# Kernel tuning notes

Measured on AMD Instinct MI355X. Metric: run time of the kernel, lower is better.

## Reference

```python
import jax, jax.numpy as jnp
import numpy as np

B, S, H, E, V, OOV = 64, 400, 512, 256, 50000, 100

def setup_inputs() -> dict:
    key = jax.random.key(0)
    ks = jax.random.split(key, 32)
    p = lambda i, shape: jax.random.normal(ks[i], shape, jnp.float32) * 0.02
    emb = p(0, (V, E)).at[0].set(0.0)  # padding_idx=0
    return dict(
        summaries_in=jax.random.randint(ks[1], (B,), 1, V),
        h0=jax.random.normal(ks[2], (B, H), jnp.float32),
        c0=jax.random.normal(ks[3], (B, H), jnp.float32),
        encoder_out=jax.random.normal(ks[4], (B, S, 2 * H), jnp.float32),
        encoder_features=jax.random.normal(ks[5], (S * B, 2 * H), jnp.float32),
        encoder_mask=jnp.ones((S, B), jnp.float32),
        context=jax.random.normal(ks[6], (B, 2 * H), jnp.float32),
        coverage=jax.random.uniform(ks[7], (S, B), jnp.float32) * 0.01,
        texts_extended=jax.random.randint(ks[8], (S, B), 0, V + OOV),
        oov_size=OOV,
        emb=emb,
        W_feat=p(10, (2 * H, 2 * H)), b_feat=p(11, (2 * H,)),
        W_cov=p(12, (2 * H,)), b_cov=p(13, (2 * H,)),
        w_att=p(14, (2 * H,)), b_att=p(15, ()),
        W_ih=p(16, (4 * H, E)), W_hh=p(17, (4 * H, H)),
        b_ih=p(18, (4 * H,)), b_hh=p(19, (4 * H,)),
        W_ctx=p(20, (E, 2 * H + E)), b_ctx=p(21, (E,)),
        W_pg=p(22, (4 * H + E,)), b_pg=p(23, ()),
        W_o1=p(24, (H, 3 * H)), b_o1=p(25, (H,)),
        W_o2=p(26, (V, H)), b_o2=p(27, (V,)),
    )


def reference(summaries_in, h0, c0, encoder_out, encoder_features, encoder_mask,
              context, coverage, texts_extended, oov_size, emb,
              W_feat, b_feat, W_cov, b_cov, w_att, b_att,
              W_ih, W_hh, b_ih, b_hh, W_ctx, b_ctx, W_pg, b_pg,
              W_o1, b_o1, W_o2, b_o2):
    # embedding + context projection: [B, 2H+E] -> [B, E]
    x = emb[summaries_in]
    ctx_out = jnp.concatenate([context, x], axis=1) @ W_ctx.T + b_ctx
    # single LSTM step (torch gate order i, f, g, o)
    gates = ctx_out @ W_ih.T + b_ih + h0 @ W_hh.T + b_hh
    i, f, g, o = jnp.split(gates, 4, axis=1)
    c = jax.nn.sigmoid(f) * c0 + jax.nn.sigmoid(i) * jnp.tanh(g)
    h = jax.nn.sigmoid(o) * jnp.tanh(c)
    hidden_out = jnp.concatenate([h, c], axis=1)  # [B, 2H]
    # Bahdanau attention with coverage
    dec_feat = hidden_out @ W_feat.T + b_feat                 # [B, 2H]
    ef = encoder_features.reshape(S, B, 2 * H)                # [S, B, 2H]
    cov_feat = coverage[..., None] * W_cov + b_cov            # Linear(1, 2H)
    e = jnp.tanh(ef + dec_feat[None] + cov_feat) @ w_att + b_att  # [S, B]
    a = jax.nn.softmax(e, axis=0) * encoder_mask
    a = a / jnp.sum(a, axis=0, keepdims=True)                 # renormalize (Normalize(0))
    ctx_new = jnp.einsum('sb,bsd->bd', a, encoder_out)        # [B, 2H]
    coverage_next = coverage + a
    # pointer-generator mix
    gen_in = jnp.concatenate([ctx_new, hidden_out, ctx_out], axis=1)  # [B, 4H+E]
    p_gen = jax.nn.sigmoid(gen_in @ W_pg + b_pg)[:, None]             # [B, 1]
    logits = (jnp.concatenate([h, ctx_new], axis=1) @ W_o1.T + b_o1) @ W_o2.T + b_o2
    vocab_dist = p_gen * jax.nn.softmax(logits, axis=1)       # [B, V]
    attn_w = (1.0 - p_gen) * a.T                              # [B, S]
    vd = jnp.concatenate([vocab_dist, jnp.zeros((B, oov_size), vocab_dist.dtype)], axis=1)
    vd = vd.at[jnp.arange(B)[:, None], texts_extended.T].add(attn_w)  # scatter_add copy dist
    return vd, hidden_out, ctx_new, a, coverage_next
```

## Files before the change

kernel.cpp:

```cpp
#include <hip/hip_runtime.h>
#include <cmath>

#define B 64
#define S 400
#define H 512
#define E 256
#define V 50000
#define OOV 100
#define H2 1024
#define VDN (V + OOV)
#define NBLK_V 782
#define SC 8

typedef __attribute__((ext_vector_type(8))) short short8;
typedef __attribute__((ext_vector_type(4))) float f32x4;

__device__ __forceinline__ float wred_sum(float v) {
#pragma unroll
  for (int o = 32; o > 0; o >>= 1) v += __shfl_down(v, o, 64);
  return v;
}
__device__ __forceinline__ float wred_max(float v) {
#pragma unroll
  for (int o = 32; o > 0; o >>= 1) v = fmaxf(v, __shfl_down(v, o, 64));
  return v;
}
__device__ __forceinline__ short f2bf(float f) {
  return __builtin_bit_cast(short, (__bf16)f);
}
__device__ __forceinline__ float ftanh(float x) {
  float e = __expf(2.f * x);
  return 1.f - 2.f * __builtin_amdgcn_rcpf(e + 1.f);
}
__device__ __forceinline__ float fsig(float x) {
  return __builtin_amdgcn_rcpf(1.f + __expf(-x));
}

__global__ __launch_bounds__(256) void k_pre(
    const float* __restrict__ b_ctx, const float* __restrict__ b_ih,
    const float* __restrict__ b_hh, const float* __restrict__ b_feat,
    const float* __restrict__ b_o1, const float* __restrict__ context,
    const float* __restrict__ emb, const int* __restrict__ sumin,
    const float* __restrict__ h0, float* __restrict__ ctxoutT4,
    float* __restrict__ gates, float* __restrict__ dfeat,
    float* __restrict__ innerT4, float* __restrict__ catT4,
    float* __restrict__ h0T4) {
  int idx = blockIdx.x * 256 + threadIdx.x;
  if (idx < 16384) {
    int j = ((idx >> 8) << 2) + (idx & 3);
    ctxoutT4[idx] = b_ctx[j];
  } else if (idx < 16384 + 131072) {
    int i = idx - 16384;
    int j = i & 2047;
    gates[i] = b_ih[j] + b_hh[j];
  } else if (idx < 16384 + 131072 + 65536) {
    int i = idx - 16384 - 131072;
    dfeat[i] = b_feat[i & 1023];
  } else if (idx < 245760) {
    int i = idx - 16384 - 131072 - 65536;
    int j = ((i >> 8) << 2) + (i & 3);
    innerT4[i] = b_o1[j];
  } else if (idx < 245760 + 81920) {
    int i = idx - 245760;
    int e = i & 3, b = (i >> 2) & 63, q = i >> 8;
    int k = q * 4 + e;
    catT4[i] = (k < 1024) ? context[b * 1024 + k]
                          : emb[(size_t)sumin[b] * 256 + (k - 1024)];
  } else {
    int i = idx - 245760 - 81920;
    int e = i & 3, b = (i >> 2) & 63, q = i >> 8;
    h0T4[i] = h0[b * 512 + q * 4 + e];
  }
}

template <int R, int KC, int OUTMODE>
__global__ __launch_bounds__(256) void k_gemmsk(
    const float* __restrict__ A1, const float* __restrict__ W1, int ldw1, int s1,
    const float* __restrict__ A2, const float* __restrict__ W2, int ldw2,
    float* __restrict__ out, int ldout) {
  const int lane = threadIdx.x;
  const int w = threadIdx.y;
  const int j0 = blockIdx.x * (4 * R) + w * R;
  const float* A;
  const float* W;
  int ldw, kc0;
  if ((int)blockIdx.y < s1) {
    A = A1; W = W1; ldw = ldw1; kc0 = blockIdx.y * KC;
  } else {
    A = A2; W = W2; ldw = ldw2; kc0 = (blockIdx.y - s1) * KC;
  }
  float acc[R];
#pragma unroll
  for (int r = 0; r < R; ++r) acc[r] = 0.f;
  const float* ap = A + (size_t)kc0 * 256 + lane * 4;
  const float* wr[R];
#pragma unroll
  for (int r = 0; r < R; ++r) wr[r] = W + (size_t)(j0 + r) * ldw + kc0 * 4;
#pragma unroll 8
  for (int k4 = 0; k4 < KC; ++k4) {
    float4 av = *(const float4*)(ap + (size_t)k4 * 256);
#pragma unroll
    for (int r = 0; r < R; ++r) {
      float4 wv = *(const float4*)(wr[r] + k4 * 4);
      acc[r] += av.x * wv.x + av.y * wv.y + av.z * wv.z + av.w * wv.w;
    }
  }
#pragma unroll
  for (int r = 0; r < R; ++r) {
    int j = j0 + r;
    if constexpr (OUTMODE == 0)
      atomicAdd(&out[((size_t)(j >> 2) * 64 + lane) * 4 + (j & 3)], acc[r]);
    else
      atomicAdd(&out[(size_t)lane * ldout + j], acc[r]);
  }
}

__global__ __launch_bounds__(256) void k_lstm(const float* __restrict__ gates,
                                              const float* __restrict__ c0,
                                              float* __restrict__ hidden,
                                              float* __restrict__ hcT4) {
  int idx = blockIdx.x * 256 + threadIdx.x;
  int b = idx >> 9, u = idx & 511;
  float gi = gates[(size_t)b * 2048 + u];
  float gf = gates[(size_t)b * 2048 + 512 + u];
  float gg = gates[(size_t)b * 2048 + 1024 + u];
  float go = gates[(size_t)b * 2048 + 1536 + u];
  float c = fsig(gf) * c0[(size_t)b * 512 + u] + fsig(gi) * ftanh(gg);
  float h = fsig(go) * ftanh(c);
  hidden[(size_t)b * H2 + u] = h;
  hidden[(size_t)b * H2 + 512 + u] = c;
  hcT4[((u >> 2) * 64 + b) * 4 + (u & 3)] = h;
  int k = 512 + u;
  hcT4[((k >> 2) * 64 + b) * 4 + (k & 3)] = c;
}

__global__ __launch_bounds__(256) void k_e(
    const float* __restrict__ ef, const float* __restrict__ dfeat,
    const float* __restrict__ cov, const float* __restrict__ Wcov,
    const float* __restrict__ bcov, const float* __restrict__ watt,
    const float* __restrict__ batt, float* __restrict__ e_out) {
  const int t = threadIdx.x;
  const int b = blockIdx.x & 63;
  const int q = blockIdx.x >> 6;
  float4 dv = ((const float4*)(dfeat + (size_t)b * H2))[t];
  float4 bc = ((const float4*)bcov)[t];
  float4 wc = ((const float4*)Wcov)[t];
  float4 wa = ((const float4*)watt)[t];
  const float bx = dv.x + bc.x, by = dv.y + bc.y;
  const float bz = dv.z + bc.z, bw = dv.w + bc.w;
  __shared__ float part[8][5];
#pragma unroll
  for (int i = 0; i < 8; ++i) {
    const int s = q * 8 + i;
    const int sb = s * B + b;
    const float cval = cov[sb];
    float4 ev = ((const float4*)(ef + (size_t)sb * H2))[t];
    float sum = ftanh(ev.x + bx + cval * wc.x) * wa.x +
                ftanh(ev.y + by + cval * wc.y) * wa.y +
                ftanh(ev.z + bz + cval * wc.z) * wa.z +
                ftanh(ev.w + bw + cval * wc.w) * wa.w;
    sum = wred_sum(sum);
    if ((t & 63) == 0) part[i][t >> 6] = sum;
  }
  __syncthreads();
  if (t < 8) {
    e_out[(q * 8 + t) * B + b] =
        part[t][0] + part[t][1] + part[t][2] + part[t][3] + batt[0];
  }
}

__global__ __launch_bounds__(256) void k_softctx(
    const float* __restrict__ e_ws, const float* __restrict__ mask,
    const float* __restrict__ coverage, const float* __restrict__ enc,
    float* __restrict__ a_out, float* __restrict__ cov_out,
    float* __restrict__ part) {
  const int b = blockIdx.x & 63;
  const int sc = blockIdx.x >> 6;
  const int t = threadIdx.x;
  const int lane = t & 63, w = t >> 6;
  __shared__ float red[4];
  __shared__ float aS[50];
  float e1 = e_ws[t * B + b];
  float e2 = (t < S - 256) ? e_ws[(t + 256) * B + b] : -INFINITY;
  float m = wred_max(fmaxf(e1, e2));
  if (lane == 0) red[w] = m;
  __syncthreads();
  const float M = fmaxf(fmaxf(red[0], red[1]), fmaxf(red[2], red[3]));
  __syncthreads();
  float x1 = mask[t * B + b] * __expf(e1 - M);
  float x2 = (t < S - 256) ? mask[(t + 256) * B + b] * __expf(e2 - M) : 0.f;
  float zs = wred_sum(x1 + x2);
  if (lane == 0) red[w] = zs;
  __syncthreads();
  const float Z = red[0] + red[1] + red[2] + red[3];
  const float rZ = 1.f / Z;
  if (t < 50) {
    int s = sc * 50 + t;
    float ex = mask[s * B + b] * __expf(e_ws[s * B + b] - M);
    float av = ex * rZ;
    aS[t] = av;
    a_out[s * B + b] = av;
    cov_out[s * B + b] = coverage[s * B + b] + av;
  }
  __syncthreads();
  const int d = t * 4;
  float4 acc = make_float4(0.f, 0.f, 0.f, 0.f);
#pragma unroll 10
  for (int i = 0; i < 50; ++i) {
    int s = sc * 50 + i;
    float av = aS[i];
    float4 ev = *(const float4*)(enc + ((size_t)b * S + s) * H2 + d);
    acc.x += av * ev.x;
    acc.y += av * ev.y;
    acc.z += av * ev.z;
    acc.w += av * ev.w;
  }
  *(float4*)(part + (size_t)blockIdx.x * H2 + d) = acc;
}

__global__ __launch_bounds__(256) void k_ctxpg(
    const float* __restrict__ part, const float* __restrict__ hidden,
    const float* __restrict__ ctxoutT4, const float* __restrict__ Wpg,
    const float* __restrict__ bpg, float* __restrict__ ctx_new,
    float* __restrict__ ctxT4, float* __restrict__ pgen) {
  const int b = blockIdx.x;
  const int t = threadIdx.x;
  const int lane = t & 63, w = t >> 6;
  const int d = t * 4;
  float4 s = make_float4(0.f, 0.f, 0.f, 0.f);
#pragma unroll
  for (int sc = 0; sc < SC; ++sc) {
    float4 v = *(const float4*)(part + (size_t)(sc * 64 + b) * H2 + d);
    s.x += v.x; s.y += v.y; s.z += v.z; s.w += v.w;
  }
  *(float4*)(ctx_new + (size_t)b * H2 + d) = s;
  *(float4*)(ctxT4 + (size_t)t * 256 + b * 4) = s;
  float p = s.x * Wpg[d] + s.y * Wpg[d + 1] + s.z * Wpg[d + 2] + s.w * Wpg[d + 3];
#pragma unroll
  for (int j = 0; j < 4; ++j) {
    int k = t + j * 256;
    p += hidden[(size_t)b * H2 + k] * Wpg[1024 + k];
  }
  p += ctxoutT4[(size_t)(t >> 2) * 256 + b * 4 + (t & 3)] * Wpg[2048 + t];
  p = wred_sum(p);
  __shared__ float red[4];
  if (lane == 0) red[w] = p;
  __syncthreads();
  if (t == 0) {
    float dd = red[0] + red[1] + red[2] + red[3] + bpg[0];
    pgen[b] = fsig(dd);
  }
}

__global__ __launch_bounds__(256) void k_packinner(const float* __restrict__ innerT4,
                                                   short8* __restrict__ packB) {
  int f = blockIdx.x * 256 + threadIdx.x;
  int l = f & 63, bt = (f >> 6) & 3, ks = f >> 8;
  int b = bt * 16 + (l & 15);
  int kbase = ks * 32 + (l >> 4) * 8;
  float4 q0 = *(const float4*)&innerT4[(size_t)(kbase / 4) * 256 + b * 4];
  float4 q1 = *(const float4*)&innerT4[(size_t)(kbase / 4 + 1) * 256 + b * 4];
  short8 frag;
  frag[0] = f2bf(q0.x); frag[1] = f2bf(q0.y);
  frag[2] = f2bf(q0.z); frag[3] = f2bf(q0.w);
  frag[4] = f2bf(q1.x); frag[5] = f2bf(q1.y);
  frag[6] = f2bf(q1.z); frag[7] = f2bf(q1.w);
  packB[f] = frag;
}

__global__ __launch_bounds__(256) void k_mfma_logits(
    const float* __restrict__ W2, const short8* __restrict__ packB,
    const float* __restrict__ bias, float* __restrict__ logits,
    float* __restrict__ mp, float* __restrict__ zp) {
  const int l = threadIdx.x;
  const int w = threadIdx.y;
  const int jblk = blockIdx.x * 64;
  const int jv = min(jblk + w * 16 + (l & 15), V - 1);
  const float4* wp4 = (const float4*)(W2 + (size_t)jv * 512 + (l >> 4) * 8);

  f32x4 acc0 = {0.f, 0.f, 0.f, 0.f}, acc1 = acc0, acc2 = acc0, acc3 = acc0;
  float4 cw0 = wp4[0], cw1 = wp4[1];
#pragma unroll
  for (int ks = 0; ks < 16; ++ks) {
    float4 nw0, nw1;
    if (ks < 15) { nw0 = wp4[(ks + 1) * 8]; nw1 = wp4[(ks + 1) * 8 + 1]; }
    short8 af;
    af[0] = f2bf(cw0.x); af[1] = f2bf(cw0.y); af[2] = f2bf(cw0.z); af[3] = f2bf(cw0.w);
    af[4] = f2bf(cw1.x); af[5] = f2bf(cw1.y); af[6] = f2bf(cw1.z); af[7] = f2bf(cw1.w);
    short8 b0 = packB[(ks * 4 + 0) * 64 + l];
    short8 b1 = packB[(ks * 4 + 1) * 64 + l];
    short8 b2 = packB[(ks * 4 + 2) * 64 + l];
    short8 b3 = packB[(ks * 4 + 3) * 64 + l];
    acc0 = __builtin_amdgcn_mfma_f32_16x16x32_bf16(af, b0, acc0, 0, 0, 0);
    acc1 = __builtin_amdgcn_mfma_f32_16x16x32_bf16(af, b1, acc1, 0, 0, 0);
    acc2 = __builtin_amdgcn_mfma_f32_16x16x32_bf16(af, b2, acc2, 0, 0, 0);
    acc3 = __builtin_amdgcn_mfma_f32_16x16x32_bf16(af, b3, acc3, 0, 0, 0);
    if (ks < 15) { cw0 = nw0; cw1 = nw1; }
  }

  __shared__ float tile[64][65];
  const int rbase = w * 16 + (l >> 4) * 4;
#pragma unroll
  for (int v = 0; v < 4; ++v) {
    int jl = rbase + v;
    int j = jblk + jl;
    float bv = bias[min(j, V - 1)];
    bool valid = (j < V);
    tile[jl][0 * 16 + (l & 15)] = valid ? acc0[v] + bv : -INFINITY;
    tile[jl][1 * 16 + (l & 15)] = valid ? acc1[v] + bv : -INFINITY;
    tile[jl][2 * 16 + (l & 15)] = valid ? acc2[v] + bv : -INFINITY;
    tile[jl][3 * 16 + (l & 15)] = valid ? acc3[v] + bv : -INFINITY;
  }
  __syncthreads();
  const int t = w * 64 + l;
#pragma unroll
  for (int i = 0; i < 16; ++i) {
    int idx = i * 256 + t;
    int jl = idx & 63;
    int b = idx >> 6;
    int j = jblk + jl;
    if (j < V) logits[(size_t)b * V + j] = tile[jl][b];
  }
  if (t < 64) {
    float m = -INFINITY;
#pragma unroll
    for (int jl = 0; jl < 64; ++jl) m = fmaxf(m, tile[jl][t]);
    float z = 0.f;
#pragma unroll
    for (int jl = 0; jl < 64; ++jl) z += __expf(tile[jl][t] - m);
    mp[(size_t)blockIdx.x * 64 + t] = m;
    zp[(size_t)blockIdx.x * 64 + t] = z;
  }
}

__global__ __launch_bounds__(256) void k_vdms(
    const float* __restrict__ logits, const float* __restrict__ mp,
    const float* __restrict__ zp, const float* __restrict__ pgen,
    const float* __restrict__ a_out, const int* __restrict__ tex,
    float* __restrict__ out) {
  const int b = blockIdx.x >> 3;
  const int c = blockIdx.x & 7;
  const int t = threadIdx.x;
  const int lane = t & 63, w = t >> 6;
  __shared__ float red[4];
  __shared__ float hist[6272];
  float m = -INFINITY;
  for (int i = t; i < NBLK_V; i += 256) m = fmaxf(m, mp[i * 64 + b]);
  m = wred_max(m);
  if (lane == 0) red[w] = m;
  __syncthreads();
  const float M = fmaxf(fmaxf(red[0], red[1]), fmaxf(red[2], red[3]));
  __syncthreads();
  float z = 0.f;
  for (int i = t; i < NBLK_V; i += 256) z += zp[i * 64 + b] * __expf(mp[i * 64 + b] - M);
  z = wred_sum(z);
  if (lane == 0) red[w] = z;
  __syncthreads();
  const float Z = red[0] + red[1] + red[2] + red[3];
  const float pg = pgen[b];
  const float scale = pg / Z;
  const float wq = 1.f - pg;
  const int v0 = c * 6272;
  const int v1 = min(v0 + 6272, VDN);
  for (int i = t; i < 6272; i += 256) hist[i] = 0.f;
  __syncthreads();
  for (int s = t; s < S; s += 256) {
    int v = tex[s * B + b];
    if (v >= v0 && v < v1) atomicAdd(&hist[v - v0], wq * a_out[s * B + b]);
  }
  __syncthreads();
  for (int v = v0 + t; v < v1; v += 256) {
    float val = (v < V) ? scale * __expf(logits[(size_t)b * V + v] - M) : 0.f;
    out[(size_t)b * VDN + v] = val + hist[v - v0];
  }
}

extern "C" void kernel_launch(void* const* d_in, const int* in_sizes, int n_in,
                              void* d_out, int out_size, void* d_ws, size_t ws_size,
                              hipStream_t stream) {
  const int* sumin = (const int*)d_in[0];
  const float* h0 = (const float*)d_in[1];
  const float* c0 = (const float*)d_in[2];
  const float* enc_out = (const float*)d_in[3];
  const float* ef = (const float*)d_in[4];
  const float* mask = (const float*)d_in[5];
  const float* context = (const float*)d_in[6];
  const float* coverage = (const float*)d_in[7];
  const int* tex = (const int*)d_in[8];
  const float* emb = (const float*)d_in[10];
  const float* W_feat = (const float*)d_in[11];
  const float* b_feat = (const float*)d_in[12];
  const float* W_cov = (const float*)d_in[13];
  const float* b_cov = (const float*)d_in[14];
  const float* w_att = (const float*)d_in[15];
  const float* b_att = (const float*)d_in[16];
  const float* W_ih = (const float*)d_in[17];
  const float* W_hh = (const float*)d_in[18];
  const float* b_ih = (const float*)d_in[19];
  const float* b_hh = (const float*)d_in[20];
  const float* W_ctx = (const float*)d_in[21];
  const float* b_ctx = (const float*)d_in[22];
  const float* W_pg = (const float*)d_in[23];
  const float* b_pg = (const float*)d_in[24];
  const float* W_o1 = (const float*)d_in[25];
  const float* b_o1 = (const float*)d_in[26];
  const float* W_o2 = (const float*)d_in[27];
  const float* b_o2 = (const float*)d_in[28];

  float* out = (float*)d_out;
  float* vd = out;
  float* hidden = vd + (size_t)B * VDN;
  float* ctx_new = hidden + (size_t)B * H2;
  float* a_out = ctx_new + (size_t)B * H2;
  float* cov_out = a_out + (size_t)S * B;

  float* ws = (float*)d_ws;
  float* catT4 = ws;
  float* h0T4 = catT4 + 81920;
  float* ctxoutT4 = h0T4 + 32768;
  float* gates = ctxoutT4 + 16384;
  float* hidcatT4 = gates + 131072;
  float* dfeat = hidcatT4 + 65536;
  float* e_ws = dfeat + 65536;
  float* ctxnewT4 = e_ws + 25600;
  float* innerT4 = ctxnewT4 + 65536;
  float* pgen = innerT4 + 32768;
  float* mp = pgen + 64;
  float* zp = mp + 50048;
  float* packBf = zp + 50048;
  float* logits = packBf + 16384;
  float* part = logits;
  short8* packB = (short8*)packBf;

  dim3 gblk(64, 4);

  k_pre<<<1408, 256, 0, stream>>>(b_ctx, b_ih, b_hh, b_feat, b_o1, context, emb,
                                  sumin, h0, ctxoutT4, gates, dfeat, innerT4,
                                  catT4, h0T4);
  k_gemmsk<2, 64, 0><<<dim3(32, 5), gblk, 0, stream>>>(
      catT4, W_ctx, 1280, 5, nullptr, nullptr, 0, ctxoutT4, 0);
  k_gemmsk<2, 64, 1><<<dim3(256, 3), gblk, 0, stream>>>(
      ctxoutT4, W_ih, 256, 1, h0T4, W_hh, 512, gates, 2048);
  k_lstm<<<128, 256, 0, stream>>>(gates, c0, hidden, hidcatT4);
  k_gemmsk<2, 64, 1><<<dim3(128, 4), gblk, 0, stream>>>(
      hidcatT4, W_feat, 1024, 4, nullptr, nullptr, 0, dfeat, 1024);
  k_e<<<50 * 64, 256, 0, stream>>>(ef, dfeat, coverage, W_cov, b_cov, w_att,
                                   b_att, e_ws);
  k_softctx<<<SC * B, 256, 0, stream>>>(e_ws, mask, coverage, enc_out, a_out,
                                        cov_out, part);
  k_ctxpg<<<B, 256, 0, stream>>>(part, hidden, ctxoutT4, W_pg, b_pg, ctx_new,
                                 ctxnewT4, pgen);
  k_gemmsk<2, 64, 0><<<dim3(64, 6), gblk, 0, stream>>>(
      hidcatT4, W_o1, 1536, 2, ctxnewT4, W_o1 + 512, 1536, innerT4, 0);
  k_packinner<<<16, 256, 0, stream>>>(innerT4, packB);
  k_mfma_logits<<<NBLK_V, gblk, 0, stream>>>(W_o2, packB, b_o2, logits, mp, zp);
  k_vdms<<<B * 8, 256, 0, stream>>>(logits, mp, zp, pgen, a_out, tex, vd);
}
```

Before: 206.5 us.

## Store logits in bf16 and fuse softmax exp/sum into attention score kernel

The logits intermediate buffer is now stored as bf16 instead of fp32, halving the write and re-read traffic between the logits GEMM and the final vocab-distribution kernel. The attention score kernel now computes exp(e) times mask directly and accumulates the per-batch normaliser with an atomic add, so the softmax-context kernel no longer does max and sum reductions over all positions. k_e also loads all eight encoder-feature rows before computing, to expose more memory parallelism. Risks: dropping the max subtraction can overflow exp for large scores, the atomic sum is order-nondeterministic, and bf16 logits lose precision in the vocab softmax.

```diff
diff --git a/kernel.cpp b/kernel.cpp
--- a/kernel.cpp
+++ b/kernel.cpp
@@ -28,6 +28,10 @@
 __device__ __forceinline__ short f2bf(float f) {
   return __builtin_bit_cast(short, (__bf16)f);
 }
+__device__ __forceinline__ float bf2f(unsigned short u) {
+  unsigned x = (unsigned)u << 16;
+  return __builtin_bit_cast(float, x);
+}
 __device__ __forceinline__ float ftanh(float x) {
   float e = __expf(2.f * x);
   return 1.f - 2.f * __builtin_amdgcn_rcpf(e + 1.f);
@@ -44,8 +48,9 @@
     const float* __restrict__ h0, float* __restrict__ ctxoutT4,
     float* __restrict__ gates, float* __restrict__ dfeat,
     float* __restrict__ innerT4, float* __restrict__ catT4,
-    float* __restrict__ h0T4) {
+    float* __restrict__ h0T4, float* __restrict__ Zb) {
   int idx = blockIdx.x * 256 + threadIdx.x;
+  if (idx < 64) Zb[idx] = 0.f;
   if (idx < 16384) {
     int j = ((idx >> 8) << 2) + (idx & 3);
     ctxoutT4[idx] = b_ctx[j];
@@ -138,7 +143,8 @@
     const float* __restrict__ ef, const float* __restrict__ dfeat,
     const float* __restrict__ cov, const float* __restrict__ Wcov,
     const float* __restrict__ bcov, const float* __restrict__ watt,
-    const float* __restrict__ batt, float* __restrict__ e_out) {
+    const float* __restrict__ batt, const float* __restrict__ mask,
+    float* __restrict__ e_x, float* __restrict__ Zb) {
   const int t = threadIdx.x;
   const int b = blockIdx.x & 63;
   const int q = blockIdx.x >> 6;
@@ -148,59 +154,56 @@
   float4 wa = ((const float4*)watt)[t];
   const float bx = dv.x + bc.x, by = dv.y + bc.y;
   const float bz = dv.z + bc.z, bw = dv.w + bc.w;
-  __shared__ float part[8][5];
+  float4 evs[8];
+  float cvals[8];
 #pragma unroll
   for (int i = 0; i < 8; ++i) {
-    const int s = q * 8 + i;
-    const int sb = s * B + b;
-    const float cval = cov[sb];
-    float4 ev = ((const float4*)(ef + (size_t)sb * H2))[t];
-    float sum = ftanh(ev.x + bx + cval * wc.x) * wa.x +
-                ftanh(ev.y + by + cval * wc.y) * wa.y +
-                ftanh(ev.z + bz + cval * wc.z) * wa.z +
-                ftanh(ev.w + bw + cval * wc.w) * wa.w;
+    const int sb = (q * 8 + i) * B + b;
+    evs[i] = ((const float4*)(ef + (size_t)sb * H2))[t];
+    cvals[i] = cov[sb];
+  }
+  __shared__ float part[8][4];
+#pragma unroll
+  for (int i = 0; i < 8; ++i) {
+    float sum = ftanh(evs[i].x + bx + cvals[i] * wc.x) * wa.x +
+                ftanh(evs[i].y + by + cvals[i] * wc.y) * wa.y +
+                ftanh(evs[i].z + bz + cvals[i] * wc.z) * wa.z +
+                ftanh(evs[i].w + bw + cvals[i] * wc.w) * wa.w;
     sum = wred_sum(sum);
     if ((t & 63) == 0) part[i][t >> 6] = sum;
   }
   __syncthreads();
-  if (t < 8) {
-    e_out[(q * 8 + t) * B + b] =
-        part[t][0] + part[t][1] + part[t][2] + part[t][3] + batt[0];
+  if (t < 64) {
+    float x = 0.f;
+    if (t < 8) {
+      int sb = (q * 8 + t) * B + b;
+      float e = part[t][0] + part[t][1] + part[t][2] + part[t][3] + batt[0];
+      x = mask[sb] * __expf(e);
+      e_x[sb] = x;
+    }
+#pragma unroll
+    for (int o = 4; o > 0; o >>= 1) x += __shfl_down(x, o, 64);
+    if (t == 0) atomicAdd(&Zb[b], x);
   }
 }
 
 __global__ __launch_bounds__(256) void k_softctx(
-    const float* __restrict__ e_ws, const float* __restrict__ mask,
+    const float* __restrict__ e_x, const float* __restrict__ Zb,
     const float* __restrict__ coverage, const float* __restrict__ enc,
     float* __restrict__ a_out, float* __restrict__ cov_out,
     float* __restrict__ part) {
   const int b = blockIdx.x & 63;
   const int sc = blockIdx.x >> 6;
   const int t = threadIdx.x;
-  const int lane = t & 63, w = t >> 6;
-  __shared__ float red[4];
   __shared__ float aS[50];
-  float e1 = e_ws[t * B + b];
-  float e2 = (t < S - 256) ? e_ws[(t + 256) * B + b] : -INFINITY;
-  float m = wred_max(fmaxf(e1, e2));
-  if (lane == 0) red[w] = m;
-  __syncthreads();
-  const float M = fmaxf(fmaxf(red[0], red[1]), fmaxf(red[2], red[3]));
-  __syncthreads();
-  float x1 = mask[t * B + b] * __expf(e1 - M);
-  float x2 = (t < S - 256) ? mask[(t + 256) * B + b] * __expf(e2 - M) : 0.f;
-  float zs = wred_sum(x1 + x2);
-  if (lane == 0) red[w] = zs;
-  __syncthreads();
-  const float Z = red[0] + red[1] + red[2] + red[3];
-  const float rZ = 1.f / Z;
+  const float rZ = 1.f / Zb[b];
   if (t < 50) {
     int s = sc * 50 + t;
-    float ex = mask[s * B + b] * __expf(e_ws[s * B + b] - M);
-    float av = ex * rZ;
+    int sb = s * B + b;
+    float av = e_x[sb] * rZ;
     aS[t] = av;
-    a_out[s * B + b] = av;
-    cov_out[s * B + b] = coverage[s * B + b] + av;
+    a_out[sb] = av;
+    cov_out[sb] = coverage[sb] + av;
   }
   __syncthreads();
   const int d = t * 4;
@@ -270,7 +273,7 @@
 
 __global__ __launch_bounds__(256) void k_mfma_logits(
     const float* __restrict__ W2, const short8* __restrict__ packB,
-    const float* __restrict__ bias, float* __restrict__ logits,
+    const float* __restrict__ bias, unsigned short* __restrict__ logits_bf,
     float* __restrict__ mp, float* __restrict__ zp) {
   const int l = threadIdx.x;
   const int w = threadIdx.y;
@@ -319,7 +322,8 @@
     int jl = idx & 63;
     int b = idx >> 6;
     int j = jblk + jl;
-    if (j < V) logits[(size_t)b * V + j] = tile[jl][b];
+    if (j < V)
+      logits_bf[(size_t)b * V + j] = (unsigned short)f2bf(tile[jl][b]);
   }
   if (t < 64) {
     float m = -INFINITY;
@@ -334,7 +338,7 @@
 }
 
 __global__ __launch_bounds__(256) void k_vdms(
-    const float* __restrict__ logits, const float* __restrict__ mp,
+    const unsigned short* __restrict__ logits_bf, const float* __restrict__ mp,
     const float* __restrict__ zp, const float* __restrict__ pgen,
     const float* __restrict__ a_out, const int* __restrict__ tex,
     float* __restrict__ out) {
@@ -370,7 +374,8 @@
   }
   __syncthreads();
   for (int v = v0 + t; v < v1; v += 256) {
-    float val = (v < V) ? scale * __expf(logits[(size_t)b * V + v] - M) : 0.f;
+    float val =
+        (v < V) ? scale * __expf(bf2f(logits_bf[(size_t)b * V + v]) - M) : 0.f;
     out[(size_t)b * VDN + v] = val + hist[v - v0];
   }
 }
@@ -421,22 +426,24 @@
   float* gates = ctxoutT4 + 16384;
   float* hidcatT4 = gates + 131072;
   float* dfeat = hidcatT4 + 65536;
-  float* e_ws = dfeat + 65536;
-  float* ctxnewT4 = e_ws + 25600;
+  float* e_x = dfeat + 65536;
+  float* ctxnewT4 = e_x + 25600;
   float* innerT4 = ctxnewT4 + 65536;
   float* pgen = innerT4 + 32768;
-  float* mp = pgen + 64;
+  float* Zb = pgen + 64;
+  float* mp = Zb + 64;
   float* zp = mp + 50048;
   float* packBf = zp + 50048;
   float* logits = packBf + 16384;
-  float* part = logits;
+  float* part = logits + 1600064;
   short8* packB = (short8*)packBf;
+  unsigned short* logits_bf = (unsigned short*)logits;
 
   dim3 gblk(64, 4);
 
   k_pre<<<1408, 256, 0, stream>>>(b_ctx, b_ih, b_hh, b_feat, b_o1, context, emb,
                                   sumin, h0, ctxoutT4, gates, dfeat, innerT4,
-                                  catT4, h0T4);
+                                  catT4, h0T4, Zb);
   k_gemmsk<2, 64, 0><<<dim3(32, 5), gblk, 0, stream>>>(
       catT4, W_ctx, 1280, 5, nullptr, nullptr, 0, ctxoutT4, 0);
   k_gemmsk<2, 64, 1><<<dim3(256, 3), gblk, 0, stream>>>(
@@ -445,14 +452,14 @@
   k_gemmsk<2, 64, 1><<<dim3(128, 4), gblk, 0, stream>>>(
       hidcatT4, W_feat, 1024, 4, nullptr, nullptr, 0, dfeat, 1024);
   k_e<<<50 * 64, 256, 0, stream>>>(ef, dfeat, coverage, W_cov, b_cov, w_att,
-                                   b_att, e_ws);
-  k_softctx<<<SC * B, 256, 0, stream>>>(e_ws, mask, coverage, enc_out, a_out,
+                                   b_att, mask, e_x, Zb);
+  k_softctx<<<SC * B, 256, 0, stream>>>(e_x, Zb, coverage, enc_out, a_out,
                                         cov_out, part);
   k_ctxpg<<<B, 256, 0, stream>>>(part, hidden, ctxoutT4, W_pg, b_pg, ctx_new,
                                  ctxnewT4, pgen);
   k_gemmsk<2, 64, 0><<<dim3(64, 6), gblk, 0, stream>>>(
       hidcatT4, W_o1, 1536, 2, ctxnewT4, W_o1 + 512, 1536, innerT4, 0);
   k_packinner<<<16, 256, 0, stream>>>(innerT4, packB);
-  k_mfma_logits<<<NBLK_V, gblk, 0, stream>>>(W_o2, packB, b_o2, logits, mp, zp);
-  k_vdms<<<B * 8, 256, 0, stream>>>(logits, mp, zp, pgen, a_out, tex, vd);
-}
+  k_mfma_logits<<<NBLK_V, gblk, 0, stream>>>(W_o2, packB, b_o2, logits_bf, mp, zp);
+  k_vdms<<<B * 8, 256, 0, stream>>>(logits_bf, mp, zp, pgen, a_out, tex, vd);
+}
```

Measured after the change: 211.3 us. +2.4%, slower.
